# Kernel optimization log

Measured on AMD Instinct MI355X. Metric: run time of the kernel, lower is better.

The kernel has to match this reference:

```python
import jax, jax.numpy as jnp
import numpy as np

B = 64; H = 28; W = 28; DIM = 384; HEADS = 12; WIN = 7; SHIFT = 3
MLP_HID = int(DIM * 4.0)
N = WIN * WIN            # tokens per window = 49
HD = DIM // HEADS        # head dim = 32
SCALE = HD ** -0.5
NW = (H // WIN) * (W // WIN)  # windows per image = 16
NREL = (2 * WIN - 1) ** 2      # relative position table size = 169


def _rel_index():
    coords = np.stack(np.meshgrid(np.arange(WIN), np.arange(WIN), indexing='ij'))  # (2,M,M)
    cf = coords.reshape(2, -1)                       # (2, N)
    rel = (cf[:, :, None] - cf[:, None, :]).transpose(1, 2, 0)  # (N, N, 2)
    rel[:, :, 0] += WIN - 1
    rel[:, :, 1] += WIN - 1
    rel[:, :, 0] *= 2 * WIN - 1
    return rel.sum(-1)  # (N, N) int

REL_IDX = jnp.asarray(_rel_index())


def _attn_mask():
    img = np.zeros((H, W))
    rid = 0
    for hs in (slice(0, -WIN), slice(-WIN, -SHIFT), slice(-SHIFT, None)):
        for ws in (slice(0, -WIN), slice(-WIN, -SHIFT), slice(-SHIFT, None)):
            img[hs, ws] = rid
            rid += 1
    win = img.reshape(H // WIN, WIN, W // WIN, WIN).transpose(0, 2, 1, 3).reshape(-1, N)  # (nW, N)
    m = win[:, None, :] - win[:, :, None]  # matches windows.unsqueeze(1) - windows.unsqueeze(2)
    return jnp.asarray(np.where(m != 0, -100.0, 0.0).astype(np.float32))  # (nW, N, N)

ATTN_MASK = _attn_mask()


def layer_norm(x, w, b, eps=1e-5):
    mu = jnp.mean(x, -1, keepdims=True)
    var = jnp.mean(jnp.square(x - mu), -1, keepdims=True)
    return (x - mu) * jax.lax.rsqrt(var + eps) * w + b


def setup_inputs() -> dict:
    key = jax.random.key(0)
    ks = jax.random.split(key, 12)
    s = DIM ** -0.5
    return {
        'x': jax.random.normal(ks[0], (B, H * W, DIM), jnp.float32),
        'norm1_w': jnp.ones((DIM,), jnp.float32),
        'norm1_b': jnp.zeros((DIM,), jnp.float32),
        'qkv_w': jax.random.normal(ks[1], (3 * DIM, DIM), jnp.float32) * s,
        'qkv_b': jnp.zeros((3 * DIM,), jnp.float32),
        'proj_w': jax.random.normal(ks[2], (DIM, DIM), jnp.float32) * s,
        'proj_b': jnp.zeros((DIM,), jnp.float32),
        'bias_table': jax.random.normal(ks[3], (NREL, HEADS), jnp.float32) * 0.02,
        'norm2_w': jnp.ones((DIM,), jnp.float32),
        'norm2_b': jnp.zeros((DIM,), jnp.float32),
        'fc1_w': jax.random.normal(ks[4], (MLP_HID, DIM), jnp.float32) * s,
        'fc1_b': jnp.zeros((MLP_HID,), jnp.float32),
        'fc2_w': jax.random.normal(ks[5], (DIM, MLP_HID), jnp.float32) * (MLP_HID ** -0.5),
        'fc2_b': jnp.zeros((DIM,), jnp.float32),
    }


def reference(x, norm1_w, norm1_b, qkv_w, qkv_b, proj_w, proj_b, bias_table,
              norm2_w, norm2_b, fc1_w, fc1_b, fc2_w, fc2_b):
    shortcut = x
    y = layer_norm(x, norm1_w, norm1_b).reshape(B, H, W, DIM)
    # cyclic shift
    y = jnp.roll(y, (-SHIFT, -SHIFT), axis=(1, 2))
    # window partition -> (B*nW, N, C)
    xw = y.reshape(B, H // WIN, WIN, W // WIN, WIN, DIM)
    xw = xw.transpose(0, 1, 3, 2, 4, 5).reshape(-1, N, DIM)
    # window attention
    qkv = xw @ qkv_w.T + qkv_b
    qkv = qkv.reshape(-1, N, 3, HEADS, HD).transpose(2, 0, 3, 1, 4)
    q, k, v = qkv[0], qkv[1], qkv[2]              # (B*nW, h, N, d)
    attn = jnp.einsum('bhnd,bhmd->bhnm', q * SCALE, k)
    bias = bias_table[REL_IDX].transpose(2, 0, 1)  # (h, N, N)
    attn = attn + bias[None]
    attn = attn.reshape(B, NW, HEADS, N, N) + ATTN_MASK[None, :, None]
    attn = jax.nn.softmax(attn.reshape(-1, HEADS, N, N), axis=-1)
    out = jnp.einsum('bhnm,bhmd->bhnd', attn, v).transpose(0, 2, 1, 3).reshape(-1, N, DIM)
    out = out @ proj_w.T + proj_b
    # window reverse
    y = out.reshape(B, H // WIN, W // WIN, WIN, WIN, DIM)
    y = y.transpose(0, 1, 3, 2, 4, 5).reshape(B, H, W, DIM)
    y = jnp.roll(y, (SHIFT, SHIFT), axis=(1, 2))
    x = shortcut + y.reshape(B, H * W, DIM)
    # MLP
    z = layer_norm(x, norm2_w, norm2_b)
    z = jax.nn.gelu(z @ fc1_w.T + fc1_b, approximate=False) @ fc2_w.T + fc2_b
    return x + z
```

## Files before the change

kernel.cpp:

```cpp
#include <hip/hip_runtime.h>


using u16 = unsigned short;
typedef __bf16 bf16x8 __attribute__((ext_vector_type(8)));
typedef float  f32x4  __attribute__((ext_vector_type(4)));

__device__ __forceinline__ float bf2f(u16 u) {
  unsigned x = ((unsigned)u) << 16; return __builtin_bit_cast(float, x);
}
__device__ __forceinline__ u16 f2bf(float f) {
  unsigned x = __builtin_bit_cast(unsigned, f);
  x += 0x7fffu + ((x >> 16) & 1u);
  return (u16)(x >> 16);
}
__device__ __forceinline__ int region3(int s) { return s < 21 ? 0 : (s < 25 ? 1 : 2); }
__device__ __forceinline__ void unpack8(uint4 u, float* d) {
  d[0] = bf2f(u.x & 0xffff); d[1] = bf2f(u.x >> 16);
  d[2] = bf2f(u.y & 0xffff); d[3] = bf2f(u.y >> 16);
  d[4] = bf2f(u.z & 0xffff); d[5] = bf2f(u.z >> 16);
  d[6] = bf2f(u.w & 0xffff); d[7] = bf2f(u.w >> 16);
}
__device__ __forceinline__ uint4 pack8f(const float* p) {
  float4 a = *(const float4*)p, b = *(const float4*)(p + 4);
  uint4 u;
  u.x = (unsigned)f2bf(a.x) | ((unsigned)f2bf(a.y) << 16);
  u.y = (unsigned)f2bf(a.z) | ((unsigned)f2bf(a.w) << 16);
  u.z = (unsigned)f2bf(b.x) | ((unsigned)f2bf(b.y) << 16);
  u.w = (unsigned)f2bf(b.z) | ((unsigned)f2bf(b.w) << 16);
  return u;
}
__device__ __forceinline__ bf16x8 ldw8(const float* p) {
  float4 a = *(const float4*)p, b = *(const float4*)(p + 4);
  bf16x8 r;
  r[0] = __builtin_bit_cast(__bf16, f2bf(a.x));
  r[1] = __builtin_bit_cast(__bf16, f2bf(a.y));
  r[2] = __builtin_bit_cast(__bf16, f2bf(a.z));
  r[3] = __builtin_bit_cast(__bf16, f2bf(a.w));
  r[4] = __builtin_bit_cast(__bf16, f2bf(b.x));
  r[5] = __builtin_bit_cast(__bf16, f2bf(b.y));
  r[6] = __builtin_bit_cast(__bf16, f2bf(b.z));
  r[7] = __builtin_bit_cast(__bf16, f2bf(b.w));
  return r;
}
__device__ __forceinline__ float gelu_f(float v) {
  float u = v * (0.7978845608028654f + 0.0356774081f * v * v);
  float e = __expf(2.f * u);
  float t = 1.f - 2.f / (e + 1.f);
  return 0.5f * v * (1.f + t);
}

__global__ __launch_bounds__(256) void repack_kernel(
    const float* __restrict__ src, u16* __restrict__ dst, int R, int K)
{
  int i = blockIdx.x * 256 + threadIdx.x;
  int n8 = (R * K) >> 3;
  if (i >= n8) return;
  int e = i * 8;
  int r = e / K, c = e - (e / K) * K;
  size_t off = ((((size_t)(r >> 4)) * (K >> 5) + (c >> 5)) << 9) + (r & 15) * 32 + (c & 31);
  *(uint4*)&dst[off] = pack8f(src + (size_t)r * K + c);
}

template<bool BF>
__global__ __launch_bounds__(256, 2) void win_attn_kernel(
    const float* __restrict__ x, const float* __restrict__ n1w, const float* __restrict__ n1b,
    const void* __restrict__ qkv_w, const float* __restrict__ qkv_b,
    const float* __restrict__ btab, float* __restrict__ out)
{
  __shared__ __align__(16) u16 xin[64 * 392];
  __shared__ __align__(16) u16 uni[9728];
  __shared__ __align__(16) u16 vt[4864];
  __shared__ float mustd[98];

  const int tid  = threadIdx.x;
  const int lane = tid & 63;
  const int wave = tid >> 6;
  const int quad = lane >> 4;
  const int r16  = lane & 15;

  const int win  = blockIdx.x;
  const int bimg = win >> 4;
  const int wi   = win & 15;
  const int wwh  = wi >> 2, www = wi & 3;

  for (int e = tid * 8; e < 15 * 392; e += 2048)
    *(uint4*)&xin[49 * 392 + e] = make_uint4(0, 0, 0, 0);
  for (int e = tid * 8; e < 9728; e += 2048)
    *(uint4*)&uni[e] = make_uint4(0, 0, 0, 0);
  for (int e = tid * 8; e < 4864; e += 2048)
    *(uint4*)&vt[e] = make_uint4(0, 0, 0, 0);

  for (int e = tid * 8; e < 49 * 384; e += 2048) {
    int r = e / 384, c = e - (e / 384) * 384;
    int i = r / 7, j = r - (r / 7) * 7;
    int h  = wwh * 7 + i + 3; if (h  >= 28) h  -= 28;
    int w2 = www * 7 + j + 3; if (w2 >= 28) w2 -= 28;
    *(uint4*)&xin[r * 392 + c] =
        pack8f(x + ((size_t)(bimg * 784 + h * 28 + w2)) * 384 + c);
  }
  __syncthreads();

  for (int r = wave; r < 49; r += 4) {
    float v[6]; float s = 0.f;
#pragma unroll
    for (int k = 0; k < 6; ++k) { v[k] = bf2f(xin[r * 392 + lane + k * 64]); s += v[k]; }
#pragma unroll
    for (int off = 32; off; off >>= 1) s += __shfl_xor(s, off);
    float mu = s * (1.f / 384.f);
    float vs = 0.f;
#pragma unroll
    for (int k = 0; k < 6; ++k) { float d = v[k] - mu; vs += d * d; }
#pragma unroll
    for (int off = 32; off; off >>= 1) vs += __shfl_xor(vs, off);
    if (lane == 0) { mustd[r] = mu; mustd[49 + r] = rsqrtf(vs * (1.f / 384.f) + 1e-5f); }
  }
  __syncthreads();

  for (int e = tid * 8; e < 49 * 384; e += 2048) {
    int r = e / 384, c = e - (e / 384) * 384;
    float mu = mustd[r], rs = mustd[49 + r];
    float v[8];
    unpack8(*(uint4*)&xin[r * 392 + c], v);
    float4 w0 = *(const float4*)(n1w + c), w1 = *(const float4*)(n1w + c + 4);
    float4 b0 = *(const float4*)(n1b + c), b1 = *(const float4*)(n1b + c + 4);
    float wv[8] = {w0.x, w0.y, w0.z, w0.w, w1.x, w1.y, w1.z, w1.w};
    float bv[8] = {b0.x, b0.y, b0.z, b0.w, b1.x, b1.y, b1.z, b1.w};
    unsigned pk[4];
#pragma unroll
    for (int i = 0; i < 4; ++i) {
      u16 a = f2bf((v[2*i]   - mu) * rs * wv[2*i]   + bv[2*i]);
      u16 b = f2bf((v[2*i+1] - mu) * rs * wv[2*i+1] + bv[2*i+1]);
      pk[i] = (unsigned)a | ((unsigned)b << 16);
    }
    *(uint4*)&xin[r * 392 + c] = make_uint4(pk[0], pk[1], pk[2], pk[3]);
  }
  __syncthreads();

  for (int hp = 0; hp < 6; ++hp) {
    f32x4 acc[4][3];
#pragma unroll
    for (int a = 0; a < 4; ++a)
#pragma unroll
      for (int c = 0; c < 3; ++c) acc[a][c] = (f32x4){0.f, 0.f, 0.f, 0.f};

    auto loadB = [&](int nt, int kt) -> bf16x8 {
      if constexpr (BF) {
        int n_noR = wave * 48 + nt * 16;
        int ftile = (n_noR >> 6) * 24 + hp * 4 + ((n_noR >> 4) & 3);
        return *(const bf16x8*)((const u16*)qkv_w +
               ((((size_t)ftile) * 12 + kt) << 9) + r16 * 32 + quad * 8);
      } else {
        int n = wave * 48 + nt * 16 + r16;
        int f = (n >> 6) * 384 + hp * 64 + (n & 63);
        return ldw8((const float*)qkv_w + (size_t)f * 384 + kt * 32 + quad * 8);
      }
    };

    bf16x8 bc[3];
#pragma unroll
    for (int nt = 0; nt < 3; ++nt) bc[nt] = loadB(nt, 0);
    for (int kt = 0; kt < 12; ++kt) {
      bf16x8 bn[3];
      if (kt < 11) {
#pragma unroll
        for (int nt = 0; nt < 3; ++nt) bn[nt] = loadB(nt, kt + 1);
      }
      bf16x8 af[4];
#pragma unroll
      for (int mt = 0; mt < 4; ++mt)
        af[mt] = *(const bf16x8*)&xin[(mt * 16 + r16) * 392 + kt * 32 + quad * 8];
#pragma unroll
      for (int nt = 0; nt < 3; ++nt)
#pragma unroll
        for (int mt = 0; mt < 4; ++mt)
          acc[mt][nt] = __builtin_amdgcn_mfma_f32_16x16x32_bf16(af[mt], bc[nt], acc[mt][nt], 0, 0, 0);
      if (kt < 11) {
#pragma unroll
        for (int nt = 0; nt < 3; ++nt) bc[nt] = bn[nt];
      }
    }
#pragma unroll
    for (int mt = 0; mt < 4; ++mt) {
#pragma unroll
      for (int nt = 0; nt < 3; ++nt) {
#pragma unroll
        for (int rg = 0; rg < 4; ++rg) {
          int row = mt * 16 + quad * 4 + rg;
          if (row < 49) {
            int n = wave * 48 + nt * 16 + r16;
            int t = n >> 6, c6 = n & 63;
            float v = acc[mt][nt][rg] + qkv_b[t * 384 + hp * 64 + c6];
            if (t == 2) vt[(c6 >> 5) * 2432 + (c6 & 31) * 76 + row] = f2bf(v);
            else        uni[row * 140 + t * 64 + c6] = f2bf(v);
          }
        }
      }
    }
    for (int e2 = tid * 4; e2 < 15 * 128; e2 += 1024) {
      int r = 49 + (e2 >> 7), c = e2 & 127;
      *(uint2*)&uni[r * 140 + c] = make_uint2(0, 0);
    }
    __syncthreads();

    {
      const int h2   = wave >> 1;
      const int half = wave & 1;
      const int head = hp * 2 + h2;
      f32x4 s[2][4];
#pragma unroll
      for (int a = 0; a < 2; ++a)
#pragma unroll
        for (int c = 0; c < 4; ++c) s[a][c] = (f32x4){0.f, 0.f, 0.f, 0.f};
      {
        bf16x8 aq[2], bk[4];
#pragma unroll
        for (int mt2 = 0; mt2 < 2; ++mt2)
          aq[mt2] = *(const bf16x8*)&uni[((half * 2 + mt2) * 16 + r16) * 140 + h2 * 32 + quad * 8];
#pragma unroll
        for (int nt = 0; nt < 4; ++nt)
          bk[nt] = *(const bf16x8*)&uni[(nt * 16 + r16) * 140 + 64 + h2 * 32 + quad * 8];
#pragma unroll
        for (int nt = 0; nt < 4; ++nt)
#pragma unroll
          for (int mt2 = 0; mt2 < 2; ++mt2)
            s[mt2][nt] = __builtin_amdgcn_mfma_f32_16x16x32_bf16(aq[mt2], bk[nt], s[mt2][nt], 0, 0, 0);
      }
      __syncthreads();

      int colv[4], rid2v[4], i2v[4], j2v[4];
#pragma unroll
      for (int nt = 0; nt < 4; ++nt) {
        int col = nt * 16 + r16; colv[nt] = col;
        int cc = col < 49 ? col : 48;
        int i2 = cc / 7, j2 = cc - i2 * 7;
        i2v[nt] = i2; j2v[nt] = j2;
        rid2v[nt] = region3(wwh * 7 + i2) * 3 + region3(www * 7 + j2);
      }
      float den[2][4];
      u16* pb = uni + h2 * 4864;
#pragma unroll
      for (int mt2 = 0; mt2 < 2; ++mt2) {
#pragma unroll
        for (int rg = 0; rg < 4; ++rg) {
          int row = (half * 2 + mt2) * 16 + quad * 4 + rg;
          int rowc = row < 49 ? row : 48;
          int qi = rowc / 7, qj = rowc - qi * 7;
          int rid1 = region3(wwh * 7 + qi) * 3 + region3(www * 7 + qj);
          float v4[4];
#pragma unroll
          for (int nt = 0; nt < 4; ++nt) {
            if (colv[nt] < 49) {
              float sv = s[mt2][nt][rg] * 0.17677669529663689f;
              sv += btab[((qi - i2v[nt] + 6) * 13 + (qj - j2v[nt] + 6)) * 12 + head];
              if (rid2v[nt] != rid1) sv -= 100.f;
              v4[nt] = sv;
            } else v4[nt] = -1e30f;
          }
          float m = fmaxf(fmaxf(v4[0], v4[1]), fmaxf(v4[2], v4[3]));
#pragma unroll
          for (int off = 1; off < 16; off <<= 1) m = fmaxf(m, __shfl_xor(m, off));
          float p[4]; float sum = 0.f;
#pragma unroll
          for (int nt = 0; nt < 4; ++nt) { p[nt] = __expf(v4[nt] - m); sum += p[nt]; }
#pragma unroll
          for (int off = 1; off < 16; off <<= 1) sum += __shfl_xor(sum, off);
          den[mt2][rg] = sum;
#pragma unroll
          for (int nt = 0; nt < 4; ++nt)
            pb[row * 76 + nt * 16 + r16] = f2bf(p[nt]);
        }
      }
      f32x4 o[2][2];
#pragma unroll
      for (int a = 0; a < 2; ++a)
#pragma unroll
        for (int c = 0; c < 2; ++c) o[a][c] = (f32x4){0.f, 0.f, 0.f, 0.f};
#pragma unroll
      for (int kc = 0; kc < 2; ++kc) {
        bf16x8 ap[2], bv[2];
#pragma unroll
        for (int mt2 = 0; mt2 < 2; ++mt2)
          ap[mt2] = *(const bf16x8*)&pb[((half * 2 + mt2) * 16 + r16) * 76 + kc * 32 + quad * 8];
#pragma unroll
        for (int nt = 0; nt < 2; ++nt)
          bv[nt] = *(const bf16x8*)&vt[h2 * 2432 + (nt * 16 + r16) * 76 + kc * 32 + quad * 8];
#pragma unroll
        for (int nt = 0; nt < 2; ++nt)
#pragma unroll
          for (int mt2 = 0; mt2 < 2; ++mt2)
            o[mt2][nt] = __builtin_amdgcn_mfma_f32_16x16x32_bf16(ap[mt2], bv[nt], o[mt2][nt], 0, 0, 0);
      }
#pragma unroll
      for (int mt2 = 0; mt2 < 2; ++mt2) {
#pragma unroll
        for (int rg = 0; rg < 4; ++rg) {
          int row = (half * 2 + mt2) * 16 + quad * 4 + rg;
          if (row < 49) {
            float inv = 1.f / den[mt2][rg];
            int qi = row / 7, qj = row - qi * 7;
            int h  = wwh * 7 + qi + 3; if (h  >= 28) h  -= 28;
            int w2 = www * 7 + qj + 3; if (w2 >= 28) w2 -= 28;
            float* orow = out + ((size_t)(bimg * 784 + h * 28 + w2)) * 384 + head * 32;
#pragma unroll
            for (int nt = 0; nt < 2; ++nt)
              orow[nt * 16 + r16] = o[mt2][nt][rg] * inv;
          }
        }
      }
    }
    __syncthreads();
  }
}

template<bool BF>
__global__ __launch_bounds__(256, 3) void proj_kernel(
    const float* attn, const void* __restrict__ proj_w, const float* __restrict__ proj_b,
    const float* __restrict__ x, float* outp)
{
  __shared__ __align__(16) u16 As[64 * 392];
  const int tid  = threadIdx.x;
  const int lane = tid & 63;
  const int wave = tid >> 6;
  const int quad = lane >> 4;
  const int r16  = lane & 15;
  const int bm   = blockIdx.x * 64;

  for (int e = tid * 8; e < 64 * 384; e += 2048) {
    int r = e / 384, c = e - (e / 384) * 384;
    *(uint4*)&As[r * 392 + c] = pack8f(attn + (size_t)(bm + r) * 384 + c);
  }
  __syncthreads();

  f32x4 acc[4][6];
#pragma unroll
  for (int a = 0; a < 4; ++a)
#pragma unroll
    for (int c = 0; c < 6; ++c) acc[a][c] = (f32x4){0.f, 0.f, 0.f, 0.f};

  auto loadB = [&](int nt, int kt) -> bf16x8 {
    if constexpr (BF) {
      return *(const bf16x8*)((const u16*)proj_w +
             ((((size_t)(wave * 6 + nt)) * 12 + kt) << 9) + r16 * 32 + quad * 8);
    } else {
      int n = wave * 96 + nt * 16 + r16;
      return ldw8((const float*)proj_w + (size_t)n * 384 + kt * 32 + quad * 8);
    }
  };

  bf16x8 bc[6];
#pragma unroll
  for (int nt = 0; nt < 6; ++nt) bc[nt] = loadB(nt, 0);
  for (int kt = 0; kt < 12; ++kt) {
    bf16x8 bn[6];
    if (kt < 11) {
#pragma unroll
      for (int nt = 0; nt < 6; ++nt) bn[nt] = loadB(nt, kt + 1);
    }
    bf16x8 af[4];
#pragma unroll
    for (int mt = 0; mt < 4; ++mt)
      af[mt] = *(const bf16x8*)&As[(mt * 16 + r16) * 392 + kt * 32 + quad * 8];
#pragma unroll
    for (int nt = 0; nt < 6; ++nt)
#pragma unroll
      for (int mt = 0; mt < 4; ++mt)
        acc[mt][nt] = __builtin_amdgcn_mfma_f32_16x16x32_bf16(af[mt], bc[nt], acc[mt][nt], 0, 0, 0);
    if (kt < 11) {
#pragma unroll
      for (int nt = 0; nt < 6; ++nt) bc[nt] = bn[nt];
    }
  }
#pragma unroll
  for (int mt = 0; mt < 4; ++mt) {
#pragma unroll
    for (int nt = 0; nt < 6; ++nt) {
#pragma unroll
      for (int rg = 0; rg < 4; ++rg) {
        int gm = bm + mt * 16 + quad * 4 + rg;
        int gn = wave * 96 + nt * 16 + r16;
        float v = acc[mt][nt][rg] + proj_b[gn] + x[(size_t)gm * 384 + gn];
        outp[(size_t)gm * 384 + gn] = v;
      }
    }
  }
}

template<bool BF>
__global__ __launch_bounds__(256, 2) void mlp_kernel(
    const float* __restrict__ n2w, const float* __restrict__ n2b,
    const void* __restrict__ fc1_w, const float* __restrict__ fc1_b,
    const void* __restrict__ fc2_w, const float* __restrict__ fc2_b,
    float* xr)
{
  __shared__ __align__(16) u16 xs[64 * 392];
  __shared__ __align__(16) u16 hs[64 * 200];
  __shared__ float mustd[128];
  const int tid  = threadIdx.x;
  const int lane = tid & 63;
  const int wave = tid >> 6;
  const int quad = lane >> 4;
  const int r16  = lane & 15;
  const int bm   = blockIdx.x * 64;

  for (int e = tid * 8; e < 64 * 384; e += 2048) {
    int r = e / 384, c = e - (e / 384) * 384;
    *(uint4*)&xs[r * 392 + c] = pack8f(xr + (size_t)(bm + r) * 384 + c);
  }
  __syncthreads();

  for (int r = wave; r < 64; r += 4) {
    float v[6]; float s = 0.f;
#pragma unroll
    for (int k = 0; k < 6; ++k) { v[k] = bf2f(xs[r * 392 + lane + k * 64]); s += v[k]; }
#pragma unroll
    for (int off = 32; off; off >>= 1) s += __shfl_xor(s, off);
    float mu = s * (1.f / 384.f);
    float vs = 0.f;
#pragma unroll
    for (int k = 0; k < 6; ++k) { float d = v[k] - mu; vs += d * d; }
#pragma unroll
    for (int off = 32; off; off >>= 1) vs += __shfl_xor(vs, off);
    if (lane == 0) { mustd[r] = mu; mustd[64 + r] = rsqrtf(vs * (1.f / 384.f) + 1e-5f); }
  }
  __syncthreads();

  for (int e = tid * 8; e < 64 * 384; e += 2048) {
    int r = e / 384, c = e - (e / 384) * 384;
    float mu = mustd[r], rs = mustd[64 + r];
    float v[8];
    unpack8(*(uint4*)&xs[r * 392 + c], v);
    float4 w0 = *(const float4*)(n2w + c), w1 = *(const float4*)(n2w + c + 4);
    float4 b0 = *(const float4*)(n2b + c), b1 = *(const float4*)(n2b + c + 4);
    float wv[8] = {w0.x, w0.y, w0.z, w0.w, w1.x, w1.y, w1.z, w1.w};
    float bv[8] = {b0.x, b0.y, b0.z, b0.w, b1.x, b1.y, b1.z, b1.w};
    unsigned pk[4];
#pragma unroll
    for (int i = 0; i < 4; ++i) {
      u16 a = f2bf((v[2*i]   - mu) * rs * wv[2*i]   + bv[2*i]);
      u16 b = f2bf((v[2*i+1] - mu) * rs * wv[2*i+1] + bv[2*i+1]);
      pk[i] = (unsigned)a | ((unsigned)b << 16);
    }
    *(uint4*)&xs[r * 392 + c] = make_uint4(pk[0], pk[1], pk[2], pk[3]);
  }
  __syncthreads();

  f32x4 acc2[4][6];
#pragma unroll
  for (int a = 0; a < 4; ++a)
#pragma unroll
    for (int c = 0; c < 6; ++c) acc2[a][c] = (f32x4){0.f, 0.f, 0.f, 0.f};

  for (int hc = 0; hc < 8; ++hc) {
    f32x4 acc1[4][3];
#pragma unroll
    for (int a = 0; a < 4; ++a)
#pragma unroll
      for (int c = 0; c < 3; ++c) acc1[a][c] = (f32x4){0.f, 0.f, 0.f, 0.f};

    auto loadB1 = [&](int nt, int kt) -> bf16x8 {
      if constexpr (BF) {
        int rt = hc * 12 + wave * 3 + nt;
        return *(const bf16x8*)((const u16*)fc1_w +
               ((((size_t)rt) * 12 + kt) << 9) + r16 * 32 + quad * 8);
      } else {
        int ng = hc * 192 + wave * 48 + nt * 16 + r16;
        return ldw8((const float*)fc1_w + (size_t)ng * 384 + kt * 32 + quad * 8);
      }
    };
    {
      bf16x8 bc[3];
#pragma unroll
      for (int nt = 0; nt < 3; ++nt) bc[nt] = loadB1(nt, 0);
      for (int kt = 0; kt < 12; ++kt) {
        bf16x8 bn[3];
        if (kt < 11) {
#pragma unroll
          for (int nt = 0; nt < 3; ++nt) bn[nt] = loadB1(nt, kt + 1);
        }
        bf16x8 af[4];
#pragma unroll
        for (int mt = 0; mt < 4; ++mt)
          af[mt] = *(const bf16x8*)&xs[(mt * 16 + r16) * 392 + kt * 32 + quad * 8];
#pragma unroll
        for (int nt = 0; nt < 3; ++nt)
#pragma unroll
          for (int mt = 0; mt < 4; ++mt)
            acc1[mt][nt] = __builtin_amdgcn_mfma_f32_16x16x32_bf16(af[mt], bc[nt], acc1[mt][nt], 0, 0, 0);
        if (kt < 11) {
#pragma unroll
          for (int nt = 0; nt < 3; ++nt) bc[nt] = bn[nt];
        }
      }
    }
    __syncthreads();
#pragma unroll
    for (int mt = 0; mt < 4; ++mt) {
#pragma unroll
      for (int nt = 0; nt < 3; ++nt) {
#pragma unroll
        for (int rg = 0; rg < 4; ++rg) {
          int row = mt * 16 + quad * 4 + rg;
          int nl  = wave * 48 + nt * 16 + r16;
          float v = acc1[mt][nt][rg] + fc1_b[hc * 192 + nl];
          hs[row * 200 + nl] = f2bf(gelu_f(v));
        }
      }
    }
    __syncthreads();
    auto loadB2 = [&](int nt, int kk) -> bf16x8 {
      if constexpr (BF) {
        int rt = wave * 6 + nt;
        return *(const bf16x8*)((const u16*)fc2_w +
               ((((size_t)rt) * 48 + hc * 6 + kk) << 9) + r16 * 32 + quad * 8);
      } else {
        int n = wave * 96 + nt * 16 + r16;
        return ldw8((const float*)fc2_w + (size_t)n * 1536 + hc * 192 + kk * 32 + quad * 8);
      }
    };
    {
      bf16x8 bc[6];
#pragma unroll
      for (int nt = 0; nt < 6; ++nt) bc[nt] = loadB2(nt, 0);
      for (int kk = 0; kk < 6; ++kk) {
        bf16x8 bn[6];
        if (kk < 5) {
#pragma unroll
          for (int nt = 0; nt < 6; ++nt) bn[nt] = loadB2(nt, kk + 1);
        }
        bf16x8 af[4];
#pragma unroll
        for (int mt = 0; mt < 4; ++mt)
          af[mt] = *(const bf16x8*)&hs[(mt * 16 + r16) * 200 + kk * 32 + quad * 8];
#pragma unroll
        for (int nt = 0; nt < 6; ++nt)
#pragma unroll
          for (int mt = 0; mt < 4; ++mt)
            acc2[mt][nt] = __builtin_amdgcn_mfma_f32_16x16x32_bf16(af[mt], bc[nt], acc2[mt][nt], 0, 0, 0);
        if (kk < 5) {
#pragma unroll
          for (int nt = 0; nt < 6; ++nt) bc[nt] = bn[nt];
        }
      }
    }
  }

#pragma unroll
  for (int mt = 0; mt < 4; ++mt) {
#pragma unroll
    for (int nt = 0; nt < 6; ++nt) {
#pragma unroll
      for (int rg = 0; rg < 4; ++rg) {
        int gm = bm + mt * 16 + quad * 4 + rg;
        int gn = wave * 96 + nt * 16 + r16;
        size_t g = (size_t)gm * 384 + gn;
        xr[g] = acc2[mt][nt][rg] + fc2_b[gn] + xr[g];
      }
    }
  }
}

extern "C" void kernel_launch(void* const* d_in, const int* in_sizes, int n_in,
                              void* d_out, int out_size, void* d_ws, size_t ws_size,
                              hipStream_t stream) {
  const float* x      = (const float*)d_in[0];
  const float* n1w    = (const float*)d_in[1];
  const float* n1b    = (const float*)d_in[2];
  const float* qkv_w  = (const float*)d_in[3];
  const float* qkv_b  = (const float*)d_in[4];
  const float* proj_w = (const float*)d_in[5];
  const float* proj_b = (const float*)d_in[6];
  const float* btab   = (const float*)d_in[7];
  const float* n2w    = (const float*)d_in[8];
  const float* n2b    = (const float*)d_in[9];
  const float* fc1_w  = (const float*)d_in[10];
  const float* fc1_b  = (const float*)d_in[11];
  const float* fc2_w  = (const float*)d_in[12];
  const float* fc2_b  = (const float*)d_in[13];

  float* dout = (float*)d_out;
  (void)in_sizes; (void)n_in; (void)out_size;

  const size_t NQ = 442368, NP = 147456, N1 = 589824, N2 = 589824;
  const size_t need = (NQ + NP + N1 + N2) * sizeof(u16);

  if (d_ws && ws_size >= need) {
    u16* wq = (u16*)d_ws;
    u16* wp = wq + NQ;
    u16* w1 = wp + NP;
    u16* w2 = w1 + N1;
    repack_kernel<<<(int)((NQ / 8 + 255) / 256), 256, 0, stream>>>(qkv_w,  wq, 1152, 384);
    repack_kernel<<<(int)((NP / 8 + 255) / 256), 256, 0, stream>>>(proj_w, wp, 384, 384);
    repack_kernel<<<(int)((N1 / 8 + 255) / 256), 256, 0, stream>>>(fc1_w,  w1, 1536, 384);
    repack_kernel<<<(int)((N2 / 8 + 255) / 256), 256, 0, stream>>>(fc2_w,  w2, 384, 1536);

    win_attn_kernel<true><<<1024, 256, 0, stream>>>(x, n1w, n1b, wq, qkv_b, btab, dout);
    proj_kernel<true><<<784, 256, 0, stream>>>(dout, wp, proj_b, x, dout);
    mlp_kernel<true><<<784, 256, 0, stream>>>(n2w, n2b, w1, fc1_b, w2, fc2_b, dout);
  } else {
    win_attn_kernel<false><<<1024, 256, 0, stream>>>(x, n1w, n1b, qkv_w, qkv_b, btab, dout);
    proj_kernel<false><<<784, 256, 0, stream>>>(dout, proj_w, proj_b, x, dout);
    mlp_kernel<false><<<784, 256, 0, stream>>>(n2w, n2b, fc1_w, fc1_b, fc2_w, fc2_b, dout);
  }
}
```

Measured before the change: 682.6 us.

## Fuse attention projection and MLP into one kernel with register residual

```diff
diff --git a/kernel.cpp b/kernel.cpp
--- a/kernel.cpp
+++ b/kernel.cpp
@@ -313,84 +313,13 @@
 }
 
 template<bool BF>
-__global__ __launch_bounds__(256, 3) void proj_kernel(
+__global__ __launch_bounds__(256, 2) void pm_kernel(
     const float* attn, const void* __restrict__ proj_w, const float* __restrict__ proj_b,
-    const float* __restrict__ x, float* outp)
-{
-  __shared__ __align__(16) u16 As[64 * 392];
-  const int tid  = threadIdx.x;
-  const int lane = tid & 63;
-  const int wave = tid >> 6;
-  const int quad = lane >> 4;
-  const int r16  = lane & 15;
-  const int bm   = blockIdx.x * 64;
-
-  for (int e = tid * 8; e < 64 * 384; e += 2048) {
-    int r = e / 384, c = e - (e / 384) * 384;
-    *(uint4*)&As[r * 392 + c] = pack8f(attn + (size_t)(bm + r) * 384 + c);
-  }
-  __syncthreads();
-
-  f32x4 acc[4][6];
-#pragma unroll
-  for (int a = 0; a < 4; ++a)
-#pragma unroll
-    for (int c = 0; c < 6; ++c) acc[a][c] = (f32x4){0.f, 0.f, 0.f, 0.f};
-
-  auto loadB = [&](int nt, int kt) -> bf16x8 {
-    if constexpr (BF) {
-      return *(const bf16x8*)((const u16*)proj_w +
-             ((((size_t)(wave * 6 + nt)) * 12 + kt) << 9) + r16 * 32 + quad * 8);
-    } else {
-      int n = wave * 96 + nt * 16 + r16;
-      return ldw8((const float*)proj_w + (size_t)n * 384 + kt * 32 + quad * 8);
-    }
-  };
-
-  bf16x8 bc[6];
-#pragma unroll
-  for (int nt = 0; nt < 6; ++nt) bc[nt] = loadB(nt, 0);
-  for (int kt = 0; kt < 12; ++kt) {
-    bf16x8 bn[6];
-    if (kt < 11) {
-#pragma unroll
-      for (int nt = 0; nt < 6; ++nt) bn[nt] = loadB(nt, kt + 1);
-    }
-    bf16x8 af[4];
-#pragma unroll
-    for (int mt = 0; mt < 4; ++mt)
-      af[mt] = *(const bf16x8*)&As[(mt * 16 + r16) * 392 + kt * 32 + quad * 8];
-#pragma unroll
-    for (int nt = 0; nt < 6; ++nt)
-#pragma unroll
-      for (int mt = 0; mt < 4; ++mt)
-        acc[mt][nt] = __builtin_amdgcn_mfma_f32_16x16x32_bf16(af[mt], bc[nt], acc[mt][nt], 0, 0, 0);
-    if (kt < 11) {
-#pragma unroll
-      for (int nt = 0; nt < 6; ++nt) bc[nt] = bn[nt];
-    }
-  }
-#pragma unroll
-  for (int mt = 0; mt < 4; ++mt) {
-#pragma unroll
-    for (int nt = 0; nt < 6; ++nt) {
-#pragma unroll
-      for (int rg = 0; rg < 4; ++rg) {
-        int gm = bm + mt * 16 + quad * 4 + rg;
-        int gn = wave * 96 + nt * 16 + r16;
-        float v = acc[mt][nt][rg] + proj_b[gn] + x[(size_t)gm * 384 + gn];
-        outp[(size_t)gm * 384 + gn] = v;
-      }
-    }
-  }
-}
-
-template<bool BF>
-__global__ __launch_bounds__(256, 2) void mlp_kernel(
+    const float* __restrict__ x,
     const float* __restrict__ n2w, const float* __restrict__ n2b,
     const void* __restrict__ fc1_w, const float* __restrict__ fc1_b,
     const void* __restrict__ fc2_w, const float* __restrict__ fc2_b,
-    float* xr)
+    float* outp)
 {
   __shared__ __align__(16) u16 xs[64 * 392];
   __shared__ __align__(16) u16 hs[64 * 200];
@@ -404,7 +333,75 @@
 
   for (int e = tid * 8; e < 64 * 384; e += 2048) {
     int r = e / 384, c = e - (e / 384) * 384;
-    *(uint4*)&xs[r * 392 + c] = pack8f(xr + (size_t)(bm + r) * 384 + c);
+    *(uint4*)&xs[r * 392 + c] = pack8f(attn + (size_t)(bm + r) * 384 + c);
+  }
+  __syncthreads();
+
+  f32x4 acc2[4][6];
+#pragma unroll
+  for (int a = 0; a < 4; ++a)
+#pragma unroll
+    for (int c = 0; c < 6; ++c) acc2[a][c] = (f32x4){0.f, 0.f, 0.f, 0.f};
+
+  auto loadBp = [&](int nt, int kt) -> bf16x8 {
+    if constexpr (BF) {
+      return *(const bf16x8*)((const u16*)proj_w +
+             ((((size_t)(wave * 6 + nt)) * 12 + kt) << 9) + r16 * 32 + quad * 8);
+    } else {
+      int n = wave * 96 + nt * 16 + r16;
+      return ldw8((const float*)proj_w + (size_t)n * 384 + kt * 32 + quad * 8);
+    }
+  };
+  {
+    bf16x8 bc[6];
+#pragma unroll
+    for (int nt = 0; nt < 6; ++nt) bc[nt] = loadBp(nt, 0);
+    for (int kt = 0; kt < 12; ++kt) {
+      bf16x8 bn[6];
+      if (kt < 11) {
+#pragma unroll
+        for (int nt = 0; nt < 6; ++nt) bn[nt] = loadBp(nt, kt + 1);
+      }
+      bf16x8 af[4];
+#pragma unroll
+      for (int mt = 0; mt < 4; ++mt)
+        af[mt] = *(const bf16x8*)&xs[(mt * 16 + r16) * 392 + kt * 32 + quad * 8];
+#pragma unroll
+      for (int nt = 0; nt < 6; ++nt)
+#pragma unroll
+        for (int mt = 0; mt < 4; ++mt)
+          acc2[mt][nt] = __builtin_amdgcn_mfma_f32_16x16x32_bf16(af[mt], bc[nt], acc2[mt][nt], 0, 0, 0);
+      if (kt < 11) {
+#pragma unroll
+        for (int nt = 0; nt < 6; ++nt) bc[nt] = bn[nt];
+      }
+    }
+  }
+#pragma unroll
+  for (int mt = 0; mt < 4; ++mt) {
+#pragma unroll
+    for (int nt = 0; nt < 6; ++nt) {
+#pragma unroll
+      for (int rg = 0; rg < 4; ++rg) {
+        int gm = bm + mt * 16 + quad * 4 + rg;
+        int gn = wave * 96 + nt * 16 + r16;
+        acc2[mt][nt][rg] += proj_b[gn] + x[(size_t)gm * 384 + gn];
+      }
+    }
+  }
+  __syncthreads();
+
+#pragma unroll
+  for (int mt = 0; mt < 4; ++mt) {
+#pragma unroll
+    for (int nt = 0; nt < 6; ++nt) {
+#pragma unroll
+      for (int rg = 0; rg < 4; ++rg) {
+        int row = mt * 16 + quad * 4 + rg;
+        int col = wave * 96 + nt * 16 + r16;
+        xs[row * 392 + col] = f2bf(acc2[mt][nt][rg]);
+      }
+    }
   }
   __syncthreads();
 
@@ -444,12 +441,6 @@
   }
   __syncthreads();
 
-  f32x4 acc2[4][6];
-#pragma unroll
-  for (int a = 0; a < 4; ++a)
-#pragma unroll
-    for (int c = 0; c < 6; ++c) acc2[a][c] = (f32x4){0.f, 0.f, 0.f, 0.f};
-
   for (int hc = 0; hc < 8; ++hc) {
     f32x4 acc1[4][3];
 #pragma unroll
@@ -552,8 +543,7 @@
       for (int rg = 0; rg < 4; ++rg) {
         int gm = bm + mt * 16 + quad * 4 + rg;
         int gn = wave * 96 + nt * 16 + r16;
-        size_t g = (size_t)gm * 384 + gn;
-        xr[g] = acc2[mt][nt][rg] + fc2_b[gn] + xr[g];
+        outp[(size_t)gm * 384 + gn] = acc2[mt][nt][rg] + fc2_b[gn];
       }
     }
   }
@@ -594,11 +584,11 @@
     repack_kernel<<<(int)((N2 / 8 + 255) / 256), 256, 0, stream>>>(fc2_w,  w2, 384, 1536);
 
     win_attn_kernel<true><<<1024, 256, 0, stream>>>(x, n1w, n1b, wq, qkv_b, btab, dout);
-    proj_kernel<true><<<784, 256, 0, stream>>>(dout, wp, proj_b, x, dout);
-    mlp_kernel<true><<<784, 256, 0, stream>>>(n2w, n2b, w1, fc1_b, w2, fc2_b, dout);
+    pm_kernel<true><<<784, 256, 0, stream>>>(dout, wp, proj_b, x,
+                                             n2w, n2b, w1, fc1_b, w2, fc2_b, dout);
   } else {
     win_attn_kernel<false><<<1024, 256, 0, stream>>>(x, n1w, n1b, qkv_w, qkv_b, btab, dout);
-    proj_kernel<false><<<784, 256, 0, stream>>>(dout, proj_w, proj_b, x, dout);
-    mlp_kernel<false><<<784, 256, 0, stream>>>(n2w, n2b, fc1_w, fc1_b, fc2_w, fc2_b, dout);
-  }
-}
+    pm_kernel<false><<<784, 256, 0, stream>>>(dout, proj_w, proj_b, x,
+                                              n2w, n2b, fc1_w, fc1_b, fc2_w, fc2_b, dout);
+  }
+}
```

Result: faster. 576.8 us (-15.5%).
